# Performance work log

Hardware: AMD Instinct MI355X
Metric: run time of the kernel (lower is better)

Reference implementation:

```python
import jax, jax.numpy as jnp
import numpy as np

NS = 48          # scalar channel multiplicity ('48x0e' input irreps)
NV = 10          # vector multiplicity ('10x1o' output irreps)
N = 20000        # nodes
E = 100000       # edges
W_NUMEL = NS * NS + NS * NV  # e3nn FullyConnectedTensorProduct weight_numel = 2784
OUT_DIM = NS + 3 * NV        # '48x0e + 10x1o' -> 78


def setup_inputs() -> dict:
    key = jax.random.key(0)
    ks = jax.random.split(key, 8)
    node_attr = jax.random.normal(ks[0], (N, NS), dtype=jnp.float32)
    edge_index = jax.random.randint(ks[1], (2, E), 0, N, dtype=jnp.int32)
    edge_attr = jax.random.normal(ks[2], (E, NS), dtype=jnp.float32)
    edge_sh = jax.random.normal(ks[3], (E, 9), dtype=jnp.float32)  # sh lmax=2: 1+3+5
    fc1_w = jax.random.normal(ks[4], (3 * NS, 3 * NS), dtype=jnp.float32) / np.float32(np.sqrt(3 * NS))
    fc1_b = jnp.zeros((3 * NS,), dtype=jnp.float32)
    fc2_w = jax.random.normal(ks[5], (3 * NS, W_NUMEL), dtype=jnp.float32) / np.float32(np.sqrt(3 * NS))
    fc2_b = jnp.zeros((W_NUMEL,), dtype=jnp.float32)
    return {"node_attr": node_attr, "edge_index": edge_index, "edge_attr": edge_attr,
            "edge_sh": edge_sh, "fc1_w": fc1_w, "fc1_b": fc1_b, "fc2_w": fc2_w, "fc2_b": fc2_b}


def reference(node_attr, edge_index, edge_attr, edge_sh, fc1_w, fc1_b, fc2_w, fc2_b):
    src, dst = edge_index[0], edge_index[1]
    # edge features = [edge_attr, src scalars, dst scalars]  (n_edge_features = 3*ns)
    ea = jnp.concatenate([edge_attr, node_attr[src, :NS], node_attr[dst, :NS]], axis=-1)
    # edge MLP -> per-edge tensor-product weights (shared_weights=False)
    h = jax.nn.relu(ea @ fc1_w + fc1_b)
    w = h @ fc2_w + fc2_b                      # [E, W_NUMEL]
    w0 = w[:, :NS * NS].reshape(E, NS, NS)     # path 0e x 0e -> 0e
    w1 = w[:, NS * NS:].reshape(E, NS, NV)     # path 0e x 1o -> 1o
    x = node_attr[dst]                         # gathered scalar node features [E, NS]
    sh0 = edge_sh[:, :1]                       # l=0 component [E,1]
    sh1 = edge_sh[:, 1:4]                      # l=1 components [E,3]
    norm = np.float32(1.0 / np.sqrt(NS))       # path fan-in normalization (mul1*mul2 = NS*1)
    out0 = jnp.einsum('ei,eik->ek', x, w0) * sh0 * norm                # [E, NS]
    out1 = jnp.einsum('ek,em->ekm', jnp.einsum('ei,eik->ek', x, w1), sh1) * norm  # [E, NV, 3]
    tp = jnp.concatenate([out0, out1.reshape(E, NV * 3)], axis=-1)     # [E, OUT_DIM]
    # scatter-mean to source nodes (reduce='mean', dim_size=N)
    summed = jax.ops.segment_sum(tp, src, num_segments=N)
    counts = jax.ops.segment_sum(jnp.ones((E, 1), tp.dtype), src, num_segments=N)
    return summed / jnp.maximum(counts, 1.0)
```

## Files before the change

kernel.cpp:

```cpp
#include <hip/hip_runtime.h>
#include <hip/hip_bf16.h>

#define NS_    48
#define NV_    10
#define N_NODE 20000
#define N_EDGE 100000
#define HID    144
#define OUTC   58
#define ODIM   78
#define TILE   64
#define NTILES 1563
#define LDE    160
#define WNUM   2784

#define PG_BLKS   1920
#define PF_BLKS   90
#define PH_BLKS   391

typedef __attribute__((ext_vector_type(8))) short bf8;
typedef __attribute__((ext_vector_type(4))) float f32x4;

__device__ __forceinline__ short f2bf(float x) {
  __hip_bfloat16 h = __float2bfloat16(x);
  union { __hip_bfloat16 b; short s; } u; u.b = h; return u.s;
}
__device__ __forceinline__ unsigned pk2(float a, float b) {
  return (unsigned)(unsigned short)f2bf(a) | ((unsigned)(unsigned short)f2bf(b) << 16);
}

__global__ void prep_all(const float* __restrict__ fc1_w, const float* __restrict__ fc2_w,
                         const float* __restrict__ fc2_b, const int* __restrict__ eidx,
                         short* __restrict__ fc1frag, short* __restrict__ gfrag,
                         int* __restrict__ cnt) {
  const int b = blockIdx.x;
  if (b < PG_BLKS) {
    int idx = b * 256 + threadIdx.x;
    int j = idx & 7, l = (idx >> 3) & 63, t = idx >> 9;
    int ks = t % 5, u = t / 5;
    int strip = u & 3, i = u >> 2;
    int k = ks * 32 + ((l >> 4) << 3) + j;
    int c = strip * 16 + (l & 15);
    float v = 0.f;
    if (c < OUTC) {
      if (k < HID)
        v = (c < NS_) ? fc2_w[k * WNUM + i * NS_ + c]
                      : fc2_w[k * WNUM + NS_ * NS_ + i * NV_ + (c - NS_)];
      else if (k == HID)
        v = (c < NS_) ? fc2_b[i * NS_ + c]
                      : fc2_b[NS_ * NS_ + i * NV_ + (c - NS_)];
    }
    gfrag[idx] = f2bf(v);
  } else if (b < PG_BLKS + PF_BLKS) {
    int idx = (b - PG_BLKS) * 256 + threadIdx.x;
    if (idx >= 9 * 5 * 512) return;
    int j = idx & 7, l = (idx >> 3) & 63, t = idx >> 9;
    int ks = t % 5, nt = t / 5;
    int k = ks * 32 + ((l >> 4) << 3) + j;
    int n = nt * 16 + (l & 15);
    fc1frag[idx] = f2bf(k < HID ? fc1_w[k * HID + n] : 0.f);
  } else {
    int e = (b - PG_BLKS - PF_BLKS) * 256 + threadIdx.x;
    if (e < N_EDGE) atomicAdd(&cnt[eidx[e]], 1);
  }
}

__global__ void k_scan1(const int* __restrict__ cnt, int* __restrict__ locexc,
                        int* __restrict__ blksum) {
  __shared__ int sh[256];
  int g = blockIdx.x * 256 + threadIdx.x;
  int v = (g < N_NODE) ? cnt[g] : 0;
  sh[threadIdx.x] = v;
  __syncthreads();
  for (int d = 1; d < 256; d <<= 1) {
    int t = (threadIdx.x >= d) ? sh[threadIdx.x - d] : 0;
    __syncthreads();
    sh[threadIdx.x] += t;
    __syncthreads();
  }
  if (g < N_NODE) locexc[g] = sh[threadIdx.x] - v;
  if (threadIdx.x == 255) blksum[blockIdx.x] = sh[255];
}

__global__ void k_scan2(const int* __restrict__ blksum, int* __restrict__ blkoff) {
  __shared__ int sh[128];
  int t = threadIdx.x;
  int v = (t < 79) ? blksum[t] : 0;
  sh[t] = v;
  __syncthreads();
  for (int d = 1; d < 128; d <<= 1) {
    int x = (t >= d) ? sh[t - d] : 0;
    __syncthreads();
    sh[t] += x;
    __syncthreads();
  }
  if (t < 79) blkoff[t] = sh[t] - v;
}

__global__ void k_scatter(const int* __restrict__ eidx, const int* __restrict__ locexc,
                          const int* __restrict__ blkoff, int* __restrict__ cursor,
                          int* __restrict__ sortedE) {
  int e = blockIdx.x * 256 + threadIdx.x;
  if (e >= N_EDGE) return;
  int s = eidx[e];
  int base = blkoff[s >> 8] + locexc[s];
  int r = atomicAdd(&cursor[s], 1);
  sortedE[base + r] = e;
}

__global__ __launch_bounds__(256, 3) void fused_edge(
    const float* __restrict__ node_attr, const int* __restrict__ eidx,
    const float* __restrict__ edge_attr, const float* __restrict__ edge_sh,
    const float* __restrict__ fc1_b, const int* __restrict__ sortedE,
    const short* __restrict__ gfrag, const short* __restrict__ fc1frag,
    float* __restrict__ out)
{
  __shared__ short EA[TILE * LDE];
  __shared__ float xT[NS_ * TILE];
  __shared__ float shs[TILE * 4];
  __shared__ int   srcs[TILE];
  __shared__ int   runStart[TILE + 1], runSrc[TILE];
  __shared__ int   nRunsSh;

  const int tid  = threadIdx.x;
  const int lane = tid & 63;
  const int wv   = tid >> 6;
  const int base = blockIdx.x * TILE;

  for (int t = tid; t < TILE * 16; t += 256) {
    int r = t >> 4, c = t & 15;
    EA[r * LDE + HID + c] = 0;
  }

  {
    const int el = tid >> 2, part = tid & 3;
    const int gi = base + el;
    const bool ev = gi < N_EDGE;
    const int e  = ev ? sortedE[gi] : 0;
    const int es = ev ? eidx[e] : 0;
    const int ed = ev ? eidx[N_EDGE + e] : 0;
    if (part == 0) {
      srcs[el] = ev ? es : -1;
      #pragma unroll
      for (int c = 0; c < 4; ++c) shs[el * 4 + c] = ev ? edge_sh[(size_t)e * 9 + c] : 0.f;
    }
    const float4* pa = (const float4*)(edge_attr + (size_t)e * NS_);
    const float4* ps = (const float4*)(node_attr + (size_t)es * NS_);
    const float4* pd = (const float4*)(node_attr + (size_t)ed * NS_);
    const float4 z4 = make_float4(0.f, 0.f, 0.f, 0.f);
    #pragma unroll
    for (int q = 0; q < 3; ++q) {
      const int c0 = part * 12 + q * 4;
      float4 va = ev ? pa[part * 3 + q] : z4;
      float4 vs = ev ? ps[part * 3 + q] : z4;
      float4 vd = ev ? pd[part * 3 + q] : z4;
      *(uint2*)&EA[el * LDE + c0]           = make_uint2(pk2(va.x, va.y), pk2(va.z, va.w));
      *(uint2*)&EA[el * LDE + NS_ + c0]     = make_uint2(pk2(vs.x, vs.y), pk2(vs.z, vs.w));
      *(uint2*)&EA[el * LDE + 2 * NS_ + c0] = make_uint2(pk2(vd.x, vd.y), pk2(vd.z, vd.w));
      xT[(c0 + 0) * TILE + el] = vd.x;
      xT[(c0 + 1) * TILE + el] = vd.y;
      xT[(c0 + 2) * TILE + el] = vd.z;
      xT[(c0 + 3) * TILE + el] = vd.w;
    }
  }
  __syncthreads();

  {
    const int mrow = lane & 15;
    const int koff = (lane >> 4) << 3;
    bf8 aF[5];
    #pragma unroll
    for (int ks = 0; ks < 5; ++ks)
      aF[ks] = *(const bf8*)&EA[(wv * 16 + mrow) * LDE + ks * 32 + koff];
    #pragma unroll
    for (int nt = 0; nt < 9; ++nt) {
      f32x4 acc = {0.f, 0.f, 0.f, 0.f};
      #pragma unroll
      for (int ks = 0; ks < 5; ++ks) {
        bf8 bF = *(const bf8*)&fc1frag[((nt * 5 + ks) * 64 + lane) * 8];
        acc = __builtin_amdgcn_mfma_f32_16x16x32_bf16(aF[ks], bF, acc, 0, 0, 0);
      }
      const int col = nt * 16 + mrow;
      const float bb = fc1_b[col];
      #pragma unroll
      for (int r = 0; r < 4; ++r) {
        float h = acc[r] + bb;
        h = h > 0.f ? h : 0.f;
        EA[(wv * 16 + ((lane >> 4) << 2) + r) * LDE + col] = f2bf(h);
      }
    }
    if (lane < 16) EA[(wv * 16 + lane) * LDE + HID] = (short)0x3F80;
  }
  __syncthreads();

  {
    const int mrow = lane & 15;
    const int koff = (lane >> 4) << 3;
    const int g0 = (lane >> 4) << 2;

    f32x4 oacc[4];
    #pragma unroll
    for (int mt = 0; mt < 4; ++mt) oacc[mt] = (f32x4){0.f, 0.f, 0.f, 0.f};

    bf8 aF[4][5];
    #pragma unroll
    for (int mt = 0; mt < 4; ++mt)
      #pragma unroll
      for (int ks = 0; ks < 5; ++ks) {
        aF[mt][ks] = *(const bf8*)&EA[(mt * 16 + mrow) * LDE + ks * 32 + koff];
        asm volatile("" : "+v"(aF[mt][ks]));
      }
    __syncthreads();

    const short* gb = gfrag + wv * 2560 + lane * 8;
    auto loadB = [&](bf8 (&BF)[5], int i) {
      const short* p = gb + i * 10240;
      #pragma unroll
      for (int ks = 0; ks < 5; ++ks) BF[ks] = *(const bf8*)(p + ks * 512);
    };
    auto compute = [&](const bf8 (&BF)[5], int i) {
      #pragma unroll
      for (int mt = 0; mt < 4; ++mt) {
        f32x4 wi = {0.f, 0.f, 0.f, 0.f};
        #pragma unroll
        for (int ks = 0; ks < 5; ++ks)
          wi = __builtin_amdgcn_mfma_f32_16x16x32_bf16(aF[mt][ks], BF[ks], wi, 0, 0, 0);
        const float4 xs = *(const float4*)&xT[i * TILE + mt * 16 + g0];
        oacc[mt][0] += xs.x * wi[0];
        oacc[mt][1] += xs.y * wi[1];
        oacc[mt][2] += xs.z * wi[2];
        oacc[mt][3] += xs.w * wi[3];
      }
    };

    const int roff = (int)(blockIdx.x % (unsigned)NS_);
    auto rot = [&](int i) { int r = i + roff; return (r >= NS_) ? r - NS_ : r; };

    bf8 bA[5], bB[5];
    loadB(bA, rot(0));
    for (int i = 0; i < NS_; i += 2) {
      loadB(bB, rot(i + 1));
      compute(bA, rot(i));
      loadB(bA, rot((i + 2 < NS_) ? i + 2 : NS_ - 1));
      compute(bB, rot(i + 1));
    }

    float* O = (float*)EA;
    const float nrm = 0.14433756729740643f;
    const int col = wv * 16 + mrow;
    #pragma unroll
    for (int mt = 0; mt < 4; ++mt) {
      #pragma unroll
      for (int r = 0; r < 4; ++r) {
        const int row = mt * 16 + g0 + r;
        const float v = oacc[mt][r] * nrm;
        if (col < NS_) {
          O[row * 80 + col] = v * shs[row * 4 + 0];
        } else if (col < OUTC) {
          const int kp = col - NS_;
          O[row * 80 + NS_ + kp * 3 + 0] = v * shs[row * 4 + 1];
          O[row * 80 + NS_ + kp * 3 + 1] = v * shs[row * 4 + 2];
          O[row * 80 + NS_ + kp * 3 + 2] = v * shs[row * 4 + 3];
        }
      }
    }
  }
  __syncthreads();

  if (tid < 64) {
    const int s = srcs[tid];
    const bool valid = s >= 0;
    const bool head = valid && (tid == 0 || srcs[tid - 1] != s);
    const unsigned long long hm = __ballot(head);
    const unsigned long long vm = __ballot(valid);
    const int rank = __popcll(hm & ((1ull << tid) - 1ull));
    if (head) { runStart[rank] = tid; runSrc[rank] = s; }
    if (tid == 0) {
      const int nR = __popcll(hm);
      nRunsSh = nR;
      runStart[nR] = __popcll(vm);
    }
  }
  __syncthreads();

  {
    const float* O = (const float*)EA;
    const int nR = nRunsSh;
    for (int t = tid; t < nR * ODIM; t += 256) {
      const int k = t / ODIM, c = t - k * ODIM;
      const int rs = runStart[k], re = runStart[k + 1];
      float s = 0.f;
      for (int r = rs; r < re; ++r) s += O[r * 80 + c];
      atomicAdd(&out[(size_t)runSrc[k] * ODIM + c], s);
    }
  }
}

__global__ void finalize(float* __restrict__ out, const int* __restrict__ cnt) {
  int idx = blockIdx.x * 256 + threadIdx.x;
  if (idx >= N_NODE * ODIM) return;
  int n = idx / ODIM;
  out[idx] = out[idx] / fmaxf((float)cnt[n], 1.f);
}

extern "C" void kernel_launch(void* const* d_in, const int* in_sizes, int n_in,
                              void* d_out, int out_size, void* d_ws, size_t ws_size,
                              hipStream_t stream) {
  (void)in_sizes; (void)n_in; (void)out_size; (void)ws_size;
  const float* node_attr = (const float*)d_in[0];
  const int*   eidx      = (const int*)d_in[1];
  const float* edge_attr = (const float*)d_in[2];
  const float* edge_sh   = (const float*)d_in[3];
  const float* fc1_w     = (const float*)d_in[4];
  const float* fc1_b     = (const float*)d_in[5];
  const float* fc2_w     = (const float*)d_in[6];
  const float* fc2_b     = (const float*)d_in[7];
  float* out = (float*)d_out;

  char* ws = (char*)d_ws;
  short* gfrag   = (short*)(ws);
  short* fc1frag = (short*)(ws + 983040);
  int*   cnt     = (int*)(ws + 1029120);
  int*   locexc  = (int*)(ws + 1109120);
  int*   cursor  = (int*)(ws + 1189120);
  int*   blksum  = (int*)(ws + 1269120);
  int*   blkoff  = (int*)(ws + 1269632);
  int*   sortedE = (int*)(ws + 1270144);

  hipMemsetAsync(out, 0, (size_t)N_NODE * ODIM * sizeof(float), stream);
  hipMemsetAsync(cnt, 0, N_NODE * sizeof(int), stream);
  hipMemsetAsync(cursor, 0, N_NODE * sizeof(int), stream);

  prep_all<<<PG_BLKS + PF_BLKS + PH_BLKS, 256, 0, stream>>>(
      fc1_w, fc2_w, fc2_b, eidx, fc1frag, gfrag, cnt);

  k_scan1<<<(N_NODE + 255) / 256, 256, 0, stream>>>(cnt, locexc, blksum);
  k_scan2<<<1, 128, 0, stream>>>(blksum, blkoff);
  k_scatter<<<(N_EDGE + 255) / 256, 256, 0, stream>>>(eidx, locexc, blkoff, cursor, sortedE);

  fused_edge<<<NTILES, 256, 0, stream>>>(
      node_attr, eidx, edge_attr, edge_sh, fc1_b, sortedE, gfrag, fc1frag, out);

  finalize<<<(N_NODE * ODIM + 255) / 256, 256, 0, stream>>>(out, cnt);
}
```

Before: 167.0 us.

## Triple edge tile per block and stage fc2 weight slices through shared LDS

The edge tile grows from 64 to 192 edges, handled by 768-thread blocks of 12 waves. Each fc2 weight slice is now loaded cooperatively into a double-buffered LDS region, with a barrier per slice, and read by all waves. Before, each wave streamed its own slice fragments from global memory. This cuts per-block gfrag traffic from L2 by about 3x per edge. The run-segmentation ballot is extended across three waves. The cost is lower occupancy (one large block per CU), 48 block-wide barriers per tile, and coarser grid granularity, which can hurt tail balance.

```diff
diff --git a/kernel.cpp b/kernel.cpp
--- a/kernel.cpp
+++ b/kernel.cpp
@@ -8,8 +8,8 @@
 #define HID    144
 #define OUTC   58
 #define ODIM   78
-#define TILE   64
-#define NTILES 1563
+#define TILE3  192
+#define NB3    521
 #define LDE    160
 #define WNUM   2784
 
@@ -107,26 +107,27 @@
   sortedE[base + r] = e;
 }
 
-__global__ __launch_bounds__(256, 3) void fused_edge(
+__global__ __launch_bounds__(768) void fused_edge(
     const float* __restrict__ node_attr, const int* __restrict__ eidx,
     const float* __restrict__ edge_attr, const float* __restrict__ edge_sh,
     const float* __restrict__ fc1_b, const int* __restrict__ sortedE,
     const short* __restrict__ gfrag, const short* __restrict__ fc1frag,
     float* __restrict__ out)
 {
-  __shared__ short EA[TILE * LDE];
-  __shared__ float xT[NS_ * TILE];
-  __shared__ float shs[TILE * 4];
-  __shared__ int   srcs[TILE];
-  __shared__ int   runStart[TILE + 1], runSrc[TILE];
+  __shared__ __align__(16) short EA[TILE3 * LDE];
+  __shared__ float xT[NS_ * TILE3];
+  __shared__ float shs[TILE3 * 4];
+  __shared__ int   srcs[TILE3];
+  __shared__ int   runStart[TILE3 + 1], runSrc[TILE3];
+  __shared__ unsigned long long hmaskSh[3], vmaskSh[3];
   __shared__ int   nRunsSh;
 
   const int tid  = threadIdx.x;
   const int lane = tid & 63;
   const int wv   = tid >> 6;
-  const int base = blockIdx.x * TILE;
-
-  for (int t = tid; t < TILE * 16; t += 256) {
+  const int base = blockIdx.x * TILE3;
+
+  for (int t = tid; t < TILE3 * 16; t += 768) {
     int r = t >> 4, c = t & 15;
     EA[r * LDE + HID + c] = 0;
   }
@@ -156,10 +157,10 @@
       *(uint2*)&EA[el * LDE + c0]           = make_uint2(pk2(va.x, va.y), pk2(va.z, va.w));
       *(uint2*)&EA[el * LDE + NS_ + c0]     = make_uint2(pk2(vs.x, vs.y), pk2(vs.z, vs.w));
       *(uint2*)&EA[el * LDE + 2 * NS_ + c0] = make_uint2(pk2(vd.x, vd.y), pk2(vd.z, vd.w));
-      xT[(c0 + 0) * TILE + el] = vd.x;
-      xT[(c0 + 1) * TILE + el] = vd.y;
-      xT[(c0 + 2) * TILE + el] = vd.z;
-      xT[(c0 + 3) * TILE + el] = vd.w;
+      xT[(c0 + 0) * TILE3 + el] = vd.x;
+      xT[(c0 + 1) * TILE3 + el] = vd.y;
+      xT[(c0 + 2) * TILE3 + el] = vd.z;
+      xT[(c0 + 3) * TILE3 + el] = vd.w;
     }
   }
   __syncthreads();
@@ -193,9 +194,12 @@
   __syncthreads();
 
   {
-    const int mrow = lane & 15;
-    const int koff = (lane >> 4) << 3;
-    const int g0 = (lane >> 4) << 2;
+    const int mrow  = lane & 15;
+    const int koff  = (lane >> 4) << 3;
+    const int g0    = (lane >> 4) << 2;
+    const int strip = wv & 3;
+    const int third = wv >> 2;
+    const int rbase = third * 64;
 
     f32x4 oacc[4];
     #pragma unroll
@@ -206,52 +210,75 @@
     for (int mt = 0; mt < 4; ++mt)
       #pragma unroll
       for (int ks = 0; ks < 5; ++ks) {
-        aF[mt][ks] = *(const bf8*)&EA[(mt * 16 + mrow) * LDE + ks * 32 + koff];
+        aF[mt][ks] = *(const bf8*)&EA[(rbase + mt * 16 + mrow) * LDE + ks * 32 + koff];
         asm volatile("" : "+v"(aF[mt][ks]));
       }
     __syncthreads();
-
-    const short* gb = gfrag + wv * 2560 + lane * 8;
-    auto loadB = [&](bf8 (&BF)[5], int i) {
-      const short* p = gb + i * 10240;
-      #pragma unroll
-      for (int ks = 0; ks < 5; ++ks) BF[ks] = *(const bf8*)(p + ks * 512);
-    };
-    auto compute = [&](const bf8 (&BF)[5], int i) {
-      #pragma unroll
-      for (int mt = 0; mt < 4; ++mt) {
-        f32x4 wi = {0.f, 0.f, 0.f, 0.f};
-        #pragma unroll
-        for (int ks = 0; ks < 5; ++ks)
-          wi = __builtin_amdgcn_mfma_f32_16x16x32_bf16(aF[mt][ks], BF[ks], wi, 0, 0, 0);
-        const float4 xs = *(const float4*)&xT[i * TILE + mt * 16 + g0];
-        oacc[mt][0] += xs.x * wi[0];
-        oacc[mt][1] += xs.y * wi[1];
-        oacc[mt][2] += xs.z * wi[2];
-        oacc[mt][3] += xs.w * wi[3];
-      }
-    };
 
     const int roff = (int)(blockIdx.x % (unsigned)NS_);
     auto rot = [&](int i) { int r = i + roff; return (r >= NS_) ? r - NS_ : r; };
 
-    bf8 bA[5], bB[5];
-    loadB(bA, rot(0));
-    for (int i = 0; i < NS_; i += 2) {
-      loadB(bB, rot(i + 1));
-      compute(bA, rot(i));
-      loadB(bA, rot((i + 2 < NS_) ? i + 2 : NS_ - 1));
-      compute(bB, rot(i + 1));
+    short* GB = EA;
+    const bool has1 = tid < 512;
+
+    {
+      const uint4* gs = (const uint4*)(gfrag + (size_t)rot(0) * 10240);
+      uint4 s0 = gs[tid];
+      uint4 s1 = has1 ? gs[tid + 768] : s0;
+      ((uint4*)GB)[tid] = s0;
+      if (has1) ((uint4*)GB)[tid + 768] = s1;
+    }
+    __syncthreads();
+
+    int cur = 0;
+    for (int i = 0; i < NS_; ++i) {
+      const int ri = rot(i);
+
+      uint4 p0, p1;
+      const bool hasNext = (i + 1 < NS_);
+      if (hasNext) {
+        const uint4* gs = (const uint4*)(gfrag + (size_t)rot(i + 1) * 10240);
+        p0 = gs[tid];
+        if (has1) p1 = gs[tid + 768];
+      }
+
+      const short* gB = GB + cur * 10240 + strip * 2560 + lane * 8;
+      f32x4 wi[4];
+      #pragma unroll
+      for (int mt = 0; mt < 4; ++mt) wi[mt] = (f32x4){0.f, 0.f, 0.f, 0.f};
+      #pragma unroll
+      for (int ks = 0; ks < 5; ++ks) {
+        bf8 b = *(const bf8*)(gB + ks * 512);
+        #pragma unroll
+        for (int mt = 0; mt < 4; ++mt)
+          wi[mt] = __builtin_amdgcn_mfma_f32_16x16x32_bf16(aF[mt][ks], b, wi[mt], 0, 0, 0);
+      }
+      #pragma unroll
+      for (int mt = 0; mt < 4; ++mt) {
+        const float4 xs = *(const float4*)&xT[ri * TILE3 + rbase + mt * 16 + g0];
+        oacc[mt][0] += xs.x * wi[mt][0];
+        oacc[mt][1] += xs.y * wi[mt][1];
+        oacc[mt][2] += xs.z * wi[mt][2];
+        oacc[mt][3] += xs.w * wi[mt][3];
+      }
+
+      if (hasNext) {
+        uint4* db = (uint4*)(GB + (cur ^ 1) * 10240);
+        db[tid] = p0;
+        if (has1) db[tid + 768] = p1;
+      }
+      __syncthreads();
+      cur ^= 1;
     }
 
     float* O = (float*)EA;
     const float nrm = 0.14433756729740643f;
-    const int col = wv * 16 + mrow;
+    const int col = strip * 16 + mrow;
     #pragma unroll
     for (int mt = 0; mt < 4; ++mt) {
       #pragma unroll
       for (int r = 0; r < 4; ++r) {
-        const int row = mt * 16 + g0 + r;
+        const int row = rbase + mt * 16 + g0 + r;
         const float v = oacc[mt][r] * nrm;
         if (col < NS_) {
           O[row * 80 + col] = v * shs[row * 4 + 0];
@@ -266,18 +293,29 @@
   }
   __syncthreads();
 
-  if (tid < 64) {
+  if (tid < TILE3) {
     const int s = srcs[tid];
     const bool valid = s >= 0;
     const bool head = valid && (tid == 0 || srcs[tid - 1] != s);
     const unsigned long long hm = __ballot(head);
     const unsigned long long vm = __ballot(valid);
-    const int rank = __popcll(hm & ((1ull << tid) - 1ull));
+    if ((tid & 63) == 0) { hmaskSh[tid >> 6] = hm; vmaskSh[tid >> 6] = vm; }
+  }
+  __syncthreads();
+  if (tid < TILE3) {
+    const int s = srcs[tid];
+    const bool valid = s >= 0;
+    const bool head = valid && (tid == 0 || srcs[tid - 1] != s);
+    const int w = tid >> 6, l = tid & 63;
+    int rank = __popcll(hmaskSh[w] & ((1ull << l) - 1ull));
+    #pragma unroll
+    for (int ww = 0; ww < 3; ++ww)
+      if (ww < w) rank += __popcll(hmaskSh[ww]);
     if (head) { runStart[rank] = tid; runSrc[rank] = s; }
     if (tid == 0) {
-      const int nR = __popcll(hm);
+      const int nR = __popcll(hmaskSh[0]) + __popcll(hmaskSh[1]) + __popcll(hmaskSh[2]);
       nRunsSh = nR;
-      runStart[nR] = __popcll(vm);
+      runStart[nR] = __popcll(vmaskSh[0]) + __popcll(vmaskSh[1]) + __popcll(vmaskSh[2]);
     }
   }
   __syncthreads();
@@ -285,7 +323,7 @@
   {
     const float* O = (const float*)EA;
     const int nR = nRunsSh;
-    for (int t = tid; t < nR * ODIM; t += 256) {
+    for (int t = tid; t < nR * ODIM; t += 768) {
       const int k = t / ODIM, c = t - k * ODIM;
       const int rs = runStart[k], re = runStart[k + 1];
       float s = 0.f;
@@ -337,7 +375,7 @@
   k_scan2<<<1, 128, 0, stream>>>(blksum, blkoff);
   k_scatter<<<(N_EDGE + 255) / 256, 256, 0, stream>>>(eidx, locexc, blkoff, cursor, sortedE);
 
-  fused_edge<<<NTILES, 256, 0, stream>>>(
+  fused_edge<<<NB3, 768, 0, stream>>>(
       node_attr, eidx, edge_attr, edge_sh, fc1_b, sortedE, gfrag, fc1frag, out);
 
   finalize<<<(N_NODE * ODIM + 255) / 256, 256, 0, stream>>>(out, cnt);
```

New measurement: 191.8 us. 14.8% more time.
